# Optimization experiments

Measured on AMD Instinct MI355X. Metric: run time of the kernel, lower is better.

The kernel has to match this reference:

```python
import jax, jax.numpy as jnp
import numpy as np

EPS = 1e-6
LAM = 0.005


def setup_inputs() -> dict:
    key = jax.random.key(0)
    k1, k2, k3 = jax.random.split(key, 3)
    B, D, H, W, M = 16, 256, 128, 128, 4096
    z = jax.random.normal(k1, (B, D, H, W), dtype=jnp.float32)
    z_prime = jax.random.normal(k2, (B, D, H, W), dtype=jnp.float32)
    # Precomputed sampled pixel indices (flat over H*W). With randn inputs every
    # pixel passes the validity mask, so uniform sampling matches the original.
    flat_idx = jax.random.randint(k3, (B, M), 0, H * W, dtype=jnp.int32)
    return {"z": z, "z_prime": z_prime, "flat_idx": flat_idx}


def _gather_pixels(z, flat_idx):
    # z: (B, D, H, W), flat_idx: (B, M) -> (B*M, D)
    B, D, H, W = z.shape
    M = flat_idx.shape[1]
    z_flat = z.reshape(B, D, H * W)
    g = jnp.take_along_axis(z_flat, flat_idx[:, None, :], axis=2)  # (B, D, M)
    return g.transpose(0, 2, 1).reshape(B * M, D)


def _normalise(x):
    mean = jnp.mean(x, axis=0, keepdims=True)
    std = jnp.std(x, axis=0, keepdims=True, ddof=1)  # torch .std() is unbiased
    return (x - mean) / jnp.clip(std, EPS, None)


def reference(z, z_prime, flat_idx):
    D = z.shape[1]
    zm = _normalise(_gather_pixels(z, flat_idx))        # (N, D)
    zpm = _normalise(_gather_pixels(z_prime, flat_idx))  # (N, D)
    N = zm.shape[0]
    C = (zm.T @ zpm) / N                                 # (D, D)
    on_diag = jnp.diagonal(C)
    off_diag = C.reshape(-1)[1:].reshape(D - 1, D + 1)[:, :-1]
    loss = jnp.sum((1.0 - on_diag) ** 2) + LAM * jnp.sum(off_diag ** 2)
    return loss
```

## Files before the change

kernel.cpp:

```cpp
#include <hip/hip_runtime.h>
#include <hip/hip_bf16.h>

typedef short s16x8 __attribute__((ext_vector_type(8)));
typedef float f32x16 __attribute__((ext_vector_type(16)));

namespace {
constexpr int kB = 16;
constexpr int kD = 256;
constexpr int kHW = 16384;
constexpr int kM = 4096;
constexpr int kN = kB * kM;
constexpr int kWin = 512;
constexpr int kNWin = kHW / kWin;
constexpr int kNBlk = kB * kNWin;
constexpr int kKT = 16;
constexpr int kNIter = kWin / kKT;
constexpr float kLam = 0.005f;

__device__ __forceinline__ unsigned short f2bf(float f) {
    union { float f; unsigned u; } x{f};
    const unsigned r = x.u + 0x7FFFu + ((x.u >> 16) & 1u);
    return (unsigned short)(r >> 16);
}
__device__ __forceinline__ float bf2f(unsigned short h) {
    union { unsigned u; float f; } x;
    x.u = ((unsigned)h) << 16;
    return x.f;
}
}

#define BAR_SOFT()                                            \
    do {                                                      \
        asm volatile("s_waitcnt lgkmcnt(0)" ::: "memory");    \
        __builtin_amdgcn_s_barrier();                         \
    } while (0)

__global__ __launch_bounds__(256) void count_kernel(
    const int* __restrict__ flat_idx, int* __restrict__ cnt)
{
    __shared__ int h[kHW];
    const int t = threadIdx.x;
    const int b = blockIdx.x;
    for (int i = t; i < kHW; i += 256) h[i] = 0;
    __syncthreads();
    const int* bi = flat_idx + b * kM;
    for (int i = t; i < kM; i += 256) atomicAdd(&h[bi[i]], 1);
    __syncthreads();
    int* dst = cnt + b * kHW;
    for (int i = t; i < kHW; i += 256) dst[i] = h[i];
}

__global__ __launch_bounds__(512, 2) void fused_gram_kernel(
    const float* __restrict__ z, const float* __restrict__ zp,
    const int* __restrict__ cnt,
    __hip_bfloat16* __restrict__ partial, float* __restrict__ statsPart)
{
    __shared__ char smem[32768];

    const int bx = blockIdx.x;
    const int b = bx & (kB - 1);
    const int win0 = (bx >> 4) * kWin;
    const int t = threadIdx.x;
    const int w = t >> 6, lane = t & 63, l31 = lane & 31, half = lane >> 5;
    const int wr = w >> 2;
    const int wc = w & 3;
    const int rbase = t >> 2;
    const int cg = t & 3;

    const float* zb  = z  + (size_t)b * kD * kHW;
    const float* zpb = zp + (size_t)b * kD * kHW;
    const int* cb = cnt + b * kHW;

    f32x16 acc[4][2];
#pragma unroll
    for (int i = 0; i < 4; ++i)
#pragma unroll
        for (int j = 0; j < 2; ++j)
#pragma unroll
            for (int r = 0; r < 16; ++r) acc[i][j][r] = 0.f;

    float sA[2], ssA[2], sB[2], ssB[2];
#pragma unroll
    for (int q = 0; q < 2; ++q) { sA[q] = ssA[q] = sB[q] = ssB[q] = 0.f; }

    float4 va0[2], vb0[2], va1[2], vb1[2];
    int4 ci0, ci1;

#define LOAD_SET(S, kt)                                                     \
    {                                                                       \
        const int base_ = win0 + (kt) * kKT + cg * 4;                       \
        _Pragma("unroll")                                                   \
        for (int q = 0; q < 2; ++q) {                                       \
            const int row_ = rbase + 128 * q;                               \
            va##S[q] = *(const float4*)(zb  + (size_t)row_ * kHW + base_);  \
            vb##S[q] = *(const float4*)(zpb + (size_t)row_ * kHW + base_);  \
        }                                                                   \
        ci##S = *(const int4*)(cb + base_);                                 \
    }

#define CONV_SET(S, buf)                                                    \
    {                                                                       \
        char* As_ = smem + (buf) * 16384;                                   \
        char* Bs_ = As_ + 8192;                                             \
        const float cf_[4] = {(float)ci##S.x, (float)ci##S.y,               \
                              (float)ci##S.z, (float)ci##S.w};              \
        _Pragma("unroll")                                                   \
        for (int q = 0; q < 2; ++q) {                                       \
            const int row_ = rbase + 128 * q;                               \
            const float a_[4]  = {va##S[q].x, va##S[q].y, va##S[q].z, va##S[q].w}; \
            const float bb_[4] = {vb##S[q].x, vb##S[q].y, vb##S[q].z, vb##S[q].w}; \
            ushort4 pa_, pb_;                                               \
            unsigned short* pav_ = (unsigned short*)&pa_;                   \
            unsigned short* pbv_ = (unsigned short*)&pb_;                   \
            _Pragma("unroll")                                               \
            for (int j = 0; j < 4; ++j) {                                   \
                const float a2_ = a_[j] * a_[j];                            \
                const float b2_ = bb_[j] * bb_[j];                          \
                const float wb_ = cf_[j] * bb_[j];                          \
                sA[q] = fmaf(cf_[j], a_[j], sA[q]);                         \
                ssA[q] = fmaf(cf_[j], a2_, ssA[q]);                         \
                sB[q] = fmaf(cf_[j], bb_[j], sB[q]);                        \
                ssB[q] = fmaf(cf_[j], b2_, ssB[q]);                         \
                pav_[j] = f2bf(a_[j]);                                      \
                pbv_[j] = f2bf(wb_);                                        \
            }                                                               \
            const int off_ = (((cg >> 1) * 256 + row_) << 4) + ((cg & 1) << 3); \
            *(unsigned long long*)(As_ + off_) = *(unsigned long long*)&pa_; \
            *(unsigned long long*)(Bs_ + off_) = *(unsigned long long*)&pb_; \
        }                                                                   \
    }

    auto MFMA_STEP = [&](int buf) {
        const char* As = smem + buf * 16384;
        const char* Bs = As + 8192;
        s16x8 af[4], bfr[2];
#pragma unroll
        for (int rt = 0; rt < 4; ++rt) {
            const int row = 128 * wr + 32 * rt + l31;
            af[rt] = *(const s16x8*)(As + ((half * 256 + row) << 4));
        }
#pragma unroll
        for (int ct = 0; ct < 2; ++ct) {
            const int row = 64 * wc + 32 * ct + l31;
            bfr[ct] = *(const s16x8*)(Bs + ((half * 256 + row) << 4));
        }
#pragma unroll
        for (int rt = 0; rt < 4; ++rt)
#pragma unroll
            for (int ct = 0; ct < 2; ++ct)
                acc[rt][ct] = __builtin_amdgcn_mfma_f32_32x32x16_bf16(
                    af[rt], bfr[ct], acc[rt][ct], 0, 0, 0);
    };

    LOAD_SET(0, 0)
    CONV_SET(0, 0)
    LOAD_SET(1, 1)
    LOAD_SET(0, 2)
    BAR_SOFT();

    for (int kt = 0; kt < kNIter; kt += 2) {
        CONV_SET(1, 1)
        if (kt + 3 < kNIter) LOAD_SET(1, kt + 3)
        MFMA_STEP(0);
        BAR_SOFT();

        if (kt + 2 < kNIter) CONV_SET(0, 0)
        if (kt + 4 < kNIter) LOAD_SET(0, kt + 4)
        MFMA_STEP(1);
        BAR_SOFT();
    }
    __syncthreads();

    __hip_bfloat16* out = partial + (size_t)bx * (kD * kD);
#pragma unroll
    for (int rt = 0; rt < 4; ++rt)
#pragma unroll
        for (int ct = 0; ct < 2; ++ct)
#pragma unroll
            for (int r = 0; r < 16; ++r) {
                const int row = 128 * wr + 32 * rt + (r & 3) + 8 * (r >> 2) + 4 * half;
                const int col = 64 * wc + 32 * ct + l31;
                ((unsigned short*)out)[row * kD + col] = f2bf(acc[rt][ct][r]);
            }

    float* sd = (float*)smem;
#pragma unroll
    for (int q = 0; q < 2; ++q) {
        const int row = rbase + 128 * q;
        float* p = sd + (row * 4 + cg) * 4;
        p[0] = sA[q]; p[1] = ssA[q]; p[2] = sB[q]; p[3] = ssB[q];
    }
    __syncthreads();
    {
        const int row = t >> 1;
        const int pair = t & 1;
        float a0 = 0.f, a1 = 0.f;
#pragma unroll
        for (int g = 0; g < 4; ++g) {
            a0 += sd[(row * 4 + g) * 4 + 2 * pair];
            a1 += sd[(row * 4 + g) * 4 + 2 * pair + 1];
        }
        float* p = statsPart + ((size_t)bx * kD + row) * 4;
        p[2 * pair] = a0;
        p[2 * pair + 1] = a1;
    }
#undef LOAD_SET
#undef CONV_SET
}

__global__ __launch_bounds__(256) void reduce_gram_kernel(
    const __hip_bfloat16* __restrict__ partial, const float* __restrict__ statsPart,
    float* __restrict__ G, float* __restrict__ statsRed)
{
    const int d = blockIdx.x;
    const int t = threadIdx.x;
    const int eg = t & 31;
    const int cgp = t >> 5;

    float fa[8];
#pragma unroll
    for (int j = 0; j < 8; ++j) fa[j] = 0.f;
    const unsigned short* pbase = (const unsigned short*)partial + d * kD + eg * 8;
    for (int c0 = 0; c0 < kNBlk / 8; ++c0) {
        const int c = c0 * 8 + cgp;
        const s16x8 v = *(const s16x8*)(pbase + (size_t)c * (kD * kD));
#pragma unroll
        for (int j = 0; j < 8; ++j)
            fa[j] += bf2f(((const unsigned short*)&v)[j]);
    }
    __shared__ float sd[8][256];
#pragma unroll
    for (int j = 0; j < 8; ++j) sd[cgp][eg * 8 + j] = fa[j];
    __syncthreads();
    {
        const int e = t;
        float s = 0.f;
#pragma unroll
        for (int g = 0; g < 8; ++g) s += sd[g][e];
        G[d * kD + e] = s;
    }

    float x0 = 0.f, x1 = 0.f, x2 = 0.f, x3 = 0.f;
#pragma unroll
    for (int c = t; c < kNBlk; c += 256) {
        const float4 v = *(const float4*)(statsPart + ((size_t)c * kD + d) * 4);
        x0 += v.x; x1 += v.y; x2 += v.z; x3 += v.w;
    }
#pragma unroll
    for (int o = 32; o; o >>= 1) {
        x0 += __shfl_down(x0, o);
        x1 += __shfl_down(x1, o);
        x2 += __shfl_down(x2, o);
        x3 += __shfl_down(x3, o);
    }
    __shared__ float r[4][4];
    if ((t & 63) == 0) {
        r[t >> 6][0] = x0; r[t >> 6][1] = x1;
        r[t >> 6][2] = x2; r[t >> 6][3] = x3;
    }
    __syncthreads();
    if (t < 4) {
        statsRed[d * 4 + t] = r[0][t] + r[1][t] + r[2][t] + r[3][t];
    }
}

__global__ __launch_bounds__(256) void loss_kernel(
    const float* __restrict__ G, const float* __restrict__ statsRed,
    float* __restrict__ out)
{
    __shared__ float muA[kD], isA[kD], muB[kD], isB[kD];
    const int t = threadIdx.x;
    const float4 v = *(const float4*)(statsRed + t * 4);
    const float n = (float)kN;
    const float mA = v.x / n, mB = v.z / n;
    const float vA = (v.y - n * mA * mA) / (n - 1.f);
    const float vB = (v.w - n * mB * mB) / (n - 1.f);
    const float sdA = fmaxf(sqrtf(fmaxf(vA, 0.f)), 1e-6f);
    const float sdB = fmaxf(sqrtf(fmaxf(vB, 0.f)), 1e-6f);
    muA[t] = mA; isA[t] = 1.f / sdA;
    muB[t] = mB; isB[t] = 1.f / sdB;
    __syncthreads();

    float acc = 0.f;
    for (int d = 0; d < kD; ++d) {
        const int e = t;
        const float c = (G[d * kD + e] / n - muA[d] * muB[e]) * isA[d] * isB[e];
        if (d == e) { const float u = 1.f - c; acc += u * u; }
        else        { acc += kLam * c * c; }
    }
#pragma unroll
    for (int o = 32; o; o >>= 1) acc += __shfl_down(acc, o);
    __shared__ float r[4];
    if ((t & 63) == 0) r[t >> 6] = acc;
    __syncthreads();
    if (t == 0) out[0] = r[0] + r[1] + r[2] + r[3];
}

extern "C" void kernel_launch(void* const* d_in, const int* in_sizes, int n_in,
                              void* d_out, int out_size, void* d_ws, size_t ws_size,
                              hipStream_t stream) {
    const float* z  = (const float*)d_in[0];
    const float* zp = (const float*)d_in[1];
    const int* flat_idx = (const int*)d_in[2];
    float* out = (float*)d_out;

    char* ws = (char*)d_ws;
    int* cnt = (int*)ws;
    float* statsPart = (float*)(ws + (size_t)1 * 1024 * 1024);
    float* statsRed  = (float*)(ws + (size_t)3 * 1024 * 1024);
    float* G = (float*)(ws + (size_t)3 * 1024 * 1024 + 64 * 1024);
    __hip_bfloat16* partial = (__hip_bfloat16*)(ws + (size_t)16 * 1024 * 1024);

    count_kernel<<<kB, 256, 0, stream>>>(flat_idx, cnt);
    fused_gram_kernel<<<kNBlk, 512, 0, stream>>>(z, zp, cnt, partial, statsPart);
    reduce_gram_kernel<<<kD, 256, 0, stream>>>(partial, statsPart, G, statsRed);
    loss_kernel<<<1, 256, 0, stream>>>(G, statsRed, out);
}
```

Before: 176.6 us.

## Stage gram inputs through LDS with async global_load_lds triple-buffer ring

Replaces the register-prefetched global loads with direct global-to-LDS async loads (global_load_lds) into a three-slot fp32 ring, plus a separate double-buffered bf16 fragment area and an LDS copy of the count window. Each iteration waits on vmcnt before a barrier, then issues the stage three tiles ahead, converts the next tile and runs the MFMAs. The window per block doubles, halving the number of partial Gram matrices the reduce kernel has to sum. The cost is about 132KB of LDS per block, which limits occupancy to one block per CU and drops the 2-blocks launch bound. The grid also halves to 256 blocks, so the fp32 staging layout may hit LDS bank conflicts.

Result: slower. 200.2 us (+13.4%).

```diff
diff --git a/kernel.cpp b/kernel.cpp
--- a/kernel.cpp
+++ b/kernel.cpp
@@ -10,13 +10,18 @@
 constexpr int kHW = 16384;
 constexpr int kM = 4096;
 constexpr int kN = kB * kM;
-constexpr int kWin = 512;
+constexpr int kWin = 1024;
 constexpr int kNWin = kHW / kWin;
 constexpr int kNBlk = kB * kNWin;
 constexpr int kKT = 16;
 constexpr int kNIter = kWin / kKT;
 constexpr float kLam = 0.005f;
 
+constexpr int kLdsRing = 32768;
+constexpr int kLdsFrag = 98304;
+constexpr int kLdsCnt  = 131072;
+constexpr int kLdsTot  = 135168;
+
 __device__ __forceinline__ unsigned short f2bf(float f) {
     union { float f; unsigned u; } x{f};
     const unsigned r = x.u + 0x7FFFu + ((x.u >> 16) & 1u);
@@ -28,12 +33,6 @@
     return x.f;
 }
 }
-
-#define BAR_SOFT()                                            \
-    do {                                                      \
-        asm volatile("s_waitcnt lgkmcnt(0)" ::: "memory");    \
-        __builtin_amdgcn_s_barrier();                         \
-    } while (0)
 
 __global__ __launch_bounds__(256) void count_kernel(
     const int* __restrict__ flat_idx, int* __restrict__ cnt)
@@ -50,12 +49,12 @@
     for (int i = t; i < kHW; i += 256) dst[i] = h[i];
 }
 
-__global__ __launch_bounds__(512, 2) void fused_gram_kernel(
+__global__ __launch_bounds__(512) void fused_gram_kernel(
     const float* __restrict__ z, const float* __restrict__ zp,
     const int* __restrict__ cnt,
     __hip_bfloat16* __restrict__ partial, float* __restrict__ statsPart)
 {
-    __shared__ char smem[32768];
+    __shared__ char smem[kLdsTot];
 
     const int bx = blockIdx.x;
     const int b = bx & (kB - 1);
@@ -69,7 +68,7 @@
 
     const float* zb  = z  + (size_t)b * kD * kHW;
     const float* zpb = zp + (size_t)b * kD * kHW;
-    const int* cb = cnt + b * kHW;
+    const int* cb = cnt + b * kHW + win0;
 
     f32x16 acc[4][2];
 #pragma unroll
@@ -83,55 +82,71 @@
 #pragma unroll
     for (int q = 0; q < 2; ++q) { sA[q] = ssA[q] = sB[q] = ssB[q] = 0.f; }
 
-    float4 va0[2], vb0[2], va1[2], vb1[2];
-    int4 ci0, ci1;
-
-#define LOAD_SET(S, kt)                                                     \
-    {                                                                       \
-        const int base_ = win0 + (kt) * kKT + cg * 4;                       \
-        _Pragma("unroll")                                                   \
-        for (int q = 0; q < 2; ++q) {                                       \
-            const int row_ = rbase + 128 * q;                               \
-            va##S[q] = *(const float4*)(zb  + (size_t)row_ * kHW + base_);  \
-            vb##S[q] = *(const float4*)(zpb + (size_t)row_ * kHW + base_);  \
-        }                                                                   \
-        ci##S = *(const int4*)(cb + base_);                                 \
-    }
-
-#define CONV_SET(S, buf)                                                    \
-    {                                                                       \
-        char* As_ = smem + (buf) * 16384;                                   \
-        char* Bs_ = As_ + 8192;                                             \
-        const float cf_[4] = {(float)ci##S.x, (float)ci##S.y,               \
-                              (float)ci##S.z, (float)ci##S.w};              \
-        _Pragma("unroll")                                                   \
-        for (int q = 0; q < 2; ++q) {                                       \
-            const int row_ = rbase + 128 * q;                               \
-            const float a_[4]  = {va##S[q].x, va##S[q].y, va##S[q].z, va##S[q].w}; \
-            const float bb_[4] = {vb##S[q].x, vb##S[q].y, vb##S[q].z, vb##S[q].w}; \
-            ushort4 pa_, pb_;                                               \
-            unsigned short* pav_ = (unsigned short*)&pa_;                   \
-            unsigned short* pbv_ = (unsigned short*)&pb_;                   \
-            _Pragma("unroll")                                               \
-            for (int j = 0; j < 4; ++j) {                                   \
-                const float a2_ = a_[j] * a_[j];                            \
-                const float b2_ = bb_[j] * bb_[j];                          \
-                const float wb_ = cf_[j] * bb_[j];                          \
-                sA[q] = fmaf(cf_[j], a_[j], sA[q]);                         \
-                ssA[q] = fmaf(cf_[j], a2_, ssA[q]);                         \
-                sB[q] = fmaf(cf_[j], bb_[j], sB[q]);                        \
-                ssB[q] = fmaf(cf_[j], b2_, ssB[q]);                         \
-                pav_[j] = f2bf(a_[j]);                                      \
-                pbv_[j] = f2bf(wb_);                                        \
-            }                                                               \
-            const int off_ = (((cg >> 1) * 256 + row_) << 4) + ((cg & 1) << 3); \
-            *(unsigned long long*)(As_ + off_) = *(unsigned long long*)&pa_; \
-            *(unsigned long long*)(Bs_ + off_) = *(unsigned long long*)&pb_; \
-        }                                                                   \
-    }
-
-    auto MFMA_STEP = [&](int buf) {
-        const char* As = smem + buf * 16384;
+    auto STAGE_CNT = [&]() {
+#pragma unroll
+        for (int j = 0; j < 2; ++j) {
+            const int inst = 2 * w + j;
+            const int* gp = cb + inst * 64 + lane;
+            __builtin_amdgcn_global_load_lds(
+                (const __attribute__((address_space(1))) void*)gp,
+                (__attribute__((address_space(3))) void*)(smem + kLdsCnt + inst * 256),
+                4, 0, 0);
+        }
+    };
+
+    auto STAGE = [&](int kt) {
+        char* slot = smem + (kt % 3) * kLdsRing;
+        const int colb = win0 + kt * kKT + (lane & 3) * 4;
+#pragma unroll
+        for (int j = 0; j < 2; ++j) {
+            const int c = 2 * w + j;
+            const int row = 16 * c + (lane >> 2);
+            const float* gpA = zb  + (size_t)row * kHW + colb;
+            const float* gpB = zpb + (size_t)row * kHW + colb;
+            __builtin_amdgcn_global_load_lds(
+                (const __attribute__((address_space(1))) void*)gpA,
+                (__attribute__((address_space(3))) void*)(slot + c * 1024), 16, 0, 0);
+            __builtin_amdgcn_global_load_lds(
+                (const __attribute__((address_space(1))) void*)gpB,
+                (__attribute__((address_space(3))) void*)(slot + 16384 + c * 1024), 16, 0, 0);
+        }
+    };
+
+    auto CONV = [&](int kt) {
+        const char* Af = smem + (kt % 3) * kLdsRing;
+        const char* Bf = Af + 16384;
+        char* Ad = smem + kLdsFrag + (kt & 1) * 16384;
+        char* Bd = Ad + 8192;
+        const int4 ci = *(const int4*)(smem + kLdsCnt + ((kt * 16 + cg * 4) << 2));
+        const float cf[4] = {(float)ci.x, (float)ci.y, (float)ci.z, (float)ci.w};
+#pragma unroll
+        for (int q = 0; q < 2; ++q) {
+            const int row = rbase + 128 * q;
+            const float4 va = *(const float4*)(Af + row * 64 + cg * 16);
+            const float4 vb = *(const float4*)(Bf + row * 64 + cg * 16);
+            const float a[4]  = {va.x, va.y, va.z, va.w};
+            const float bb[4] = {vb.x, vb.y, vb.z, vb.w};
+            ushort4 pa, pb;
+            unsigned short* pav = (unsigned short*)&pa;
+            unsigned short* pbv = (unsigned short*)&pb;
+#pragma unroll
+            for (int j = 0; j < 4; ++j) {
+                const float wbv = cf[j] * bb[j];
+                sA[q]  = fmaf(cf[j], a[j], sA[q]);
+                ssA[q] = fmaf(cf[j], a[j] * a[j], ssA[q]);
+                sB[q]  = fmaf(cf[j], bb[j], sB[q]);
+                ssB[q] = fmaf(cf[j], bb[j] * bb[j], ssB[q]);
+                pav[j] = f2bf(a[j]);
+                pbv[j] = f2bf(wbv);
+            }
+            const int off = (((cg >> 1) * 256 + row) << 4) + ((cg & 1) << 3);
+            *(unsigned long long*)(Ad + off) = *(unsigned long long*)&pa;
+            *(unsigned long long*)(Bd + off) = *(unsigned long long*)&pb;
+        }
+    };
+
+    auto MFMA_STEP = [&](int fb) {
+        const char* As = smem + kLdsFrag + fb * 16384;
         const char* Bs = As + 8192;
         s16x8 af[4], bfr[2];
 #pragma unroll
@@ -152,22 +167,27 @@
                     af[rt], bfr[ct], acc[rt][ct], 0, 0, 0);
     };
 
-    LOAD_SET(0, 0)
-    CONV_SET(0, 0)
-    LOAD_SET(1, 1)
-    LOAD_SET(0, 2)
-    BAR_SOFT();
-
-    for (int kt = 0; kt < kNIter; kt += 2) {
-        CONV_SET(1, 1)
-        if (kt + 3 < kNIter) LOAD_SET(1, kt + 3)
-        MFMA_STEP(0);
-        BAR_SOFT();
-
-        if (kt + 2 < kNIter) CONV_SET(0, 0)
-        if (kt + 4 < kNIter) LOAD_SET(0, kt + 4)
-        MFMA_STEP(1);
-        BAR_SOFT();
+    STAGE_CNT();
+    STAGE(0);
+    asm volatile("s_waitcnt vmcnt(0)" ::: "memory");
+    __builtin_amdgcn_s_barrier();
+    __builtin_amdgcn_sched_barrier(0);
+    CONV(0);
+    STAGE(1);
+    STAGE(2);
+    asm volatile("s_waitcnt lgkmcnt(0)" ::: "memory");
+    __builtin_amdgcn_s_barrier();
+
+    for (int kt = 0; kt < kNIter; ++kt) {
+        if (kt <= kNIter - 3) asm volatile("s_waitcnt vmcnt(4)" ::: "memory");
+        else                  asm volatile("s_waitcnt vmcnt(0)" ::: "memory");
+        __builtin_amdgcn_s_barrier();
+        __builtin_amdgcn_sched_barrier(0);
+        if (kt + 3 < kNIter) STAGE(kt + 3);
+        if (kt + 1 < kNIter) CONV(kt + 1);
+        MFMA_STEP(kt & 1);
+        asm volatile("s_waitcnt lgkmcnt(0)" ::: "memory");
+        __builtin_amdgcn_s_barrier();
     }
     __syncthreads();
 
@@ -204,8 +224,6 @@
         p[2 * pair] = a0;
         p[2 * pair + 1] = a1;
     }
-#undef LOAD_SET
-#undef CONV_SET
 }
 
 __global__ __launch_bounds__(256) void reduce_gram_kernel(
@@ -241,10 +259,9 @@
     }
 
     float x0 = 0.f, x1 = 0.f, x2 = 0.f, x3 = 0.f;
-#pragma unroll
-    for (int c = t; c < kNBlk; c += 256) {
-        const float4 v = *(const float4*)(statsPart + ((size_t)c * kD + d) * 4);
-        x0 += v.x; x1 += v.y; x2 += v.z; x3 += v.w;
+    if (t < kNBlk) {
+        const float4 v = *(const float4*)(statsPart + ((size_t)t * kD + d) * 4);
+        x0 = v.x; x1 = v.y; x2 = v.z; x3 = v.w;
     }
 #pragma unroll
     for (int o = 32; o; o >>= 1) {
```
